# Kernel optimization log

Measured on AMD Instinct MI355X. Metric: run time of the kernel, lower is better.

Reference implementation:

```python
import jax, jax.numpy as jnp
import numpy as np

N, E, G = 30000, 240000, 1000
F, H = 78, 10            # in-features, GAT heads
HID = F * H              # 780
NEG_SLOPE = 0.2


def setup_inputs() -> dict:
    key = jax.random.key(0)
    ks = jax.random.split(key, 12)
    x = jax.random.normal(ks[0], (N, F), dtype=jnp.float32)
    edge_index = jax.random.randint(ks[1], (2, E), 0, N, dtype=jnp.int32)
    batch = jnp.sort(jax.random.randint(ks[2], (N,), 0, G, dtype=jnp.int32))
    def lin(k, fan_in, shape):
        return (jax.random.normal(k, shape, dtype=jnp.float32)
                / jnp.sqrt(jnp.float32(fan_in)))
    return {
        "x": x,
        "edge_index": edge_index,
        "batch": batch,
        "W_gat": lin(ks[3], F, (F, HID)),          # GATConv lin weight
        "att_src": lin(ks[4], F, (H, F)),          # GAT attention vectors
        "att_dst": lin(ks[5], F, (H, F)),
        "b_gat": jnp.zeros((HID,), jnp.float32),
        "W_gcn": lin(ks[6], HID, (HID, HID)),
        "b_gcn": jnp.zeros((HID,), jnp.float32),
        "W1": lin(ks[7], 2 * HID, (2 * HID, 1500)),
        "b1": jnp.zeros((1500,), jnp.float32),
        "W2": lin(ks[8], 1500, (1500, 128)),
        "b2": jnp.zeros((128,), jnp.float32),
    }


def _with_self_loops(edge_index):
    loop = jnp.arange(N, dtype=edge_index.dtype)
    src = jnp.concatenate([edge_index[0], loop])
    dst = jnp.concatenate([edge_index[1], loop])
    return src, dst


def reference(x, edge_index, batch, W_gat, att_src, att_dst, b_gat,
              W_gcn, b_gcn, W1, b1, W2, b2):
    src, dst = _with_self_loops(edge_index)  # [E+N]

    # ---- GATConv(78 -> 78, heads=10, concat) ----
    h = (x @ W_gat).reshape(N, H, F)                       # [N,H,F]
    a_src = jnp.einsum('nhf,hf->nh', h, att_src)           # [N,H]
    a_dst = jnp.einsum('nhf,hf->nh', h, att_dst)
    e = jax.nn.leaky_relu(a_src[src] + a_dst[dst], NEG_SLOPE)  # [Et,H]
    # segment softmax over incoming edges of each dst node
    e_max = jax.ops.segment_max(e, dst, num_segments=N)
    e_exp = jnp.exp(e - e_max[dst])
    denom = jax.ops.segment_sum(e_exp, dst, num_segments=N)
    alpha = e_exp / denom[dst]                             # [Et,H]
    msg = h[src] * alpha[:, :, None]                       # [Et,H,F]
    out = jax.ops.segment_sum(msg, dst, num_segments=N).reshape(N, HID) + b_gat
    out = jax.nn.relu(out)

    # ---- GCNConv(780 -> 780), symmetric norm with self loops ----
    h2 = out @ W_gcn                                       # [N,HID]
    deg = jax.ops.segment_sum(jnp.ones_like(dst, jnp.float32), dst,
                              num_segments=N)
    dinv = jax.lax.rsqrt(jnp.maximum(deg, 1.0))
    norm = dinv[src] * dinv[dst]                           # [Et]
    out2 = jax.ops.segment_sum(norm[:, None] * h2[src], dst,
                               num_segments=N) + b_gcn
    out2 = jax.nn.relu(out2)

    # ---- global mean / max pool over molecules ----
    counts = jax.ops.segment_sum(jnp.ones((N,), jnp.float32), batch,
                                 num_segments=G)
    gsum = jax.ops.segment_sum(out2, batch, num_segments=G)
    gmean = gsum / jnp.maximum(counts, 1.0)[:, None]
    gmax = jax.ops.segment_max(out2, batch, num_segments=G)
    gmax = jnp.where(counts[:, None] > 0, gmax, 0.0)
    pooled = jnp.concatenate([gmean, gmax], axis=1)        # [G, 1560]

    # ---- MLP head (dropout = identity at eval) ----
    hidfc = jax.nn.relu(pooled @ W1 + b1)
    return hidfc @ W2 + b2                                 # [G, 128]
```

## Files before the change

### kernel.cpp

```cpp
#include <hip/hip_runtime.h>

#define NN 30000
#define EE 240000
#define ET 270000
#define GG 1000
#define NH 10
#define FF 78
#define HID 780
#define NEG_SLOPE 0.2f

#define LD_H 784
#define KP_GCN 800
#define NP_HID 896
#define KP_X 96
#define MP_N 30080
#define KP_P 1600
#define NP_W1 1536
#define LD_FC 1536
#define MP_G 1024

#define MT 128
#define NT 128
#define NBLK 30
#define EB 4

#define C_X   (MP_N * KP_X)
#define C_WG  (NP_HID * KP_X)
#define C_WC  (NP_HID * KP_GCN)
#define C_W1  (NP_W1 * KP_P)
#define C_W2  (128 * LD_FC)
#define C_WS  (FF * 2 * NH)
#define C_IN  NN
#define C_TOT (C_X + C_WG + C_WC + C_W1 + C_W2 + C_WS + C_IN)

typedef __bf16 bf16_8 __attribute__((ext_vector_type(8)));
typedef float f32x4 __attribute__((ext_vector_type(4)));

__device__ __forceinline__ void async_copy16(const void* g, void* l) {
  __builtin_amdgcn_global_load_lds(
      (const __attribute__((address_space(1))) void*)g,
      (__attribute__((address_space(3))) void*)l, 16, 0, 0);
}

__device__ __forceinline__ float bf2f(unsigned int bits) {
  return __uint_as_float(bits << 16);
}

template <bool OUT_BF, int KBC, bool DBUF>
__global__ __launch_bounds__(256) void mfma_gemm(
    const __bf16* __restrict__ A, const __bf16* __restrict__ BT,
    float* __restrict__ Cf, __bf16* __restrict__ Cb,
    const float* __restrict__ bias, int M, int Kp, int Nout, int ldc,
    int relu, int rp, int nct, int mtiles) {
  constexpr int NST = KBC / 32;
  constexpr int TST = KBC / 16;
  constexpr int STAGEB = (KBC / 8) * MT * 8 * 2;
  __shared__ char smem[32768];
  int rt, ct;
  if (rp > 0) {
    int bid = blockIdx.x;
    int p = bid & 7, s = bid >> 3;
    int q = s / nct;
    rt = p * rp + q;
    ct = s - q * nct;
    if (rt >= mtiles) return;
  } else {
    rt = blockIdx.y; ct = blockIdx.x;
  }
  int row0 = rt * MT, col0 = ct * NT;
  int tid = threadIdx.x;
  int lane = tid & 63, wave = tid >> 6;
  int wm = (wave & 1) * 64, wn = (wave >> 1) * 64;
  int l15 = lane & 15, quad = lane >> 4;
  f32x4 acc[4][4] = {};

  auto stage = [&](int k0, int buf) {
    char* baseA = smem + (DBUF ? buf * 2 * STAGEB : 0);
    char* baseB = baseA + STAGEB;
    for (int t = 0; t < TST; t++) {
      int base = t * 256 + wave * 64;
      int s = base + lane;
      int kc = s >> 7, r = s & 127;
      async_copy16(A + (size_t)(row0 + r) * Kp + k0 + kc * 8,
                   baseA + (size_t)base * 16);
    }
    for (int t = 0; t < TST; t++) {
      int base = t * 256 + wave * 64;
      int s = base + lane;
      int kc = s >> 7, r = s & 127;
      async_copy16(BT + (size_t)(col0 + r) * Kp + k0 + kc * 8,
                   baseB + (size_t)base * 16);
    }
  };
  auto compute = [&](int buf) {
    char* baseA = smem + (DBUF ? buf * 2 * STAGEB : 0);
    char* baseB = baseA + STAGEB;
    for (int st = 0; st < NST; st++) {
      bf16_8 af[4], bfv[4];
      for (int mt = 0; mt < 4; mt++)
        af[mt] = *(const bf16_8*)(baseA +
            (size_t)((st * 4 + quad) * MT + wm + mt * 16 + l15) * 16);
      for (int nt = 0; nt < 4; nt++)
        bfv[nt] = *(const bf16_8*)(baseB +
            (size_t)((st * 4 + quad) * MT + wn + nt * 16 + l15) * 16);
      for (int mt = 0; mt < 4; mt++)
        for (int nt = 0; nt < 4; nt++)
          acc[mt][nt] = __builtin_amdgcn_mfma_f32_16x16x32_bf16(
              af[mt], bfv[nt], acc[mt][nt], 0, 0, 0);
    }
  };

  if (DBUF) {
    int niter = Kp / KBC;
    stage(0, 0);
    for (int k = 0; k < niter; k++) {
      __syncthreads();
      if (k + 1 < niter) stage((k + 1) * KBC, (k + 1) & 1);
      compute(k & 1);
    }
    __syncthreads();
  } else {
    for (int k0 = 0; k0 < Kp; k0 += KBC) {
      stage(k0, 0);
      __syncthreads();
      compute(0);
      __syncthreads();
    }
  }

  if (OUT_BF) {
    __bf16* Cs = (__bf16*)smem;
    for (int nt = 0; nt < 4; nt++) {
      int col_l = wn + nt * 16 + l15;
      int gcol = col0 + col_l;
      bool valid = gcol < Nout;
      float bv = (valid && bias) ? bias[gcol] : 0.f;
      int ch = col_l >> 3, wi = col_l & 7;
      for (int mt = 0; mt < 4; mt++) {
        for (int r = 0; r < 4; r++) {
          int rl = wm + mt * 16 + quad * 4 + r;
          float v = 0.f;
          if (valid) {
            v = acc[mt][nt][r] + bv;
            if (relu) v = fmaxf(v, 0.f);
          }
          Cs[rl * 128 + ((ch ^ (rl & 7)) << 3) + wi] = (__bf16)v;
        }
      }
    }
    __syncthreads();
    for (int idx = tid; idx < MT * 16; idx += 256) {
      int rl = idx >> 4, ch = idx & 15;
      int grow = row0 + rl, gcol = col0 + ch * 8;
      if (grow < M && gcol + 8 <= ldc)
        *(bf16_8*)(Cb + (size_t)grow * ldc + gcol) =
            *(const bf16_8*)&Cs[rl * 128 + ((ch ^ (rl & 7)) << 3)];
    }
  } else {
    for (int nt = 0; nt < 4; nt++) {
      int col = col0 + wn + nt * 16 + l15;
      if (col >= ldc) continue;
      bool valid = col < Nout;
      float bv = (valid && bias) ? bias[col] : 0.f;
      for (int mt = 0; mt < 4; mt++) {
        int rbase = row0 + wm + mt * 16 + quad * 4;
        for (int r = 0; r < 4; r++) {
          int row = rbase + r;
          if (row >= M) continue;
          float v = 0.f;
          if (valid) {
            v = acc[mt][nt][r] + bv;
            if (relu) v = fmaxf(v, 0.f);
          }
          Cf[(size_t)row * ldc + col] = v;
        }
      }
    }
  }
}

__global__ __launch_bounds__(256) void prep_kernel(
    const float* __restrict__ x, const float* __restrict__ W_gat,
    const float* __restrict__ att_src, const float* __restrict__ att_dst,
    const float* __restrict__ W_gcn, const float* __restrict__ W1,
    const float* __restrict__ W2, __bf16* __restrict__ x_bf,
    __bf16* __restrict__ WgatT, __bf16* __restrict__ WgcnT,
    __bf16* __restrict__ W1T, __bf16* __restrict__ W2T,
    float* __restrict__ wsd, int* __restrict__ cnt, int* __restrict__ fill,
    int* __restrict__ lo, int* __restrict__ hi) {
  int gid = blockIdx.x * 256 + threadIdx.x;
  if (gid < C_X) {
    int n = gid / KP_X, k = gid - n * KP_X;
    x_bf[gid] = (__bf16)((n < NN && k < FF) ? x[(size_t)n * FF + k] : 0.f);
    return;
  }
  gid -= C_X;
  if (gid < C_WG) {
    int n = gid / KP_X, k = gid - n * KP_X;
    WgatT[gid] = (__bf16)((n < HID && k < FF) ? W_gat[(size_t)k * HID + n] : 0.f);
    return;
  }
  gid -= C_WG;
  if (gid < C_WC) {
    int n = gid / KP_GCN, k = gid - n * KP_GCN;
    WgcnT[gid] = (__bf16)((n < HID && k < HID) ? W_gcn[(size_t)k * HID + n] : 0.f);
    return;
  }
  gid -= C_WC;
  if (gid < C_W1) {
    int n = gid / KP_P, k = gid - n * KP_P;
    W1T[gid] = (__bf16)((n < 1500 && k < 2 * HID) ? W1[(size_t)k * 1500 + n] : 0.f);
    return;
  }
  gid -= C_W1;
  if (gid < C_W2) {
    int n = gid / LD_FC, k = gid - n * LD_FC;
    W2T[gid] = (__bf16)((n < 128 && k < 1500) ? W2[(size_t)k * 128 + n] : 0.f);
    return;
  }
  gid -= C_W2;
  if (gid < C_WS) {
    int k = gid / (2 * NH), c = gid - k * (2 * NH);
    int h = (c < NH) ? c : c - NH;
    const float* att = (c < NH) ? att_src : att_dst;
    float s = 0.f;
    for (int f = 0; f < FF; f++)
      s += W_gat[(size_t)k * HID + h * FF + f] * att[h * FF + f];
    wsd[k * 2 * NH + c] = s;
    return;
  }
  gid -= C_WS;
  if (gid < C_IN) {
    cnt[gid] = 0; fill[gid] = 0;
    if (gid < GG) { lo[gid] = NN; hi[gid] = 0; }
  }
}

__device__ __forceinline__ void edge_sd(const int* __restrict__ ei, int t,
                                        int& s, int& d) {
  if (t < EE) { s = ei[t]; d = ei[EE + t]; }
  else        { s = t - EE; d = t - EE; }
}

__global__ __launch_bounds__(256) void adot_count_kernel(
    const float* __restrict__ x, const float* __restrict__ wsd,
    float* __restrict__ a_src, float* __restrict__ a_dst,
    const int* __restrict__ ei, const int* __restrict__ batch,
    int* __restrict__ cnt, int* __restrict__ lo, int* __restrict__ hi) {
  __shared__ float w_s[FF * 2 * NH];
  for (int i = threadIdx.x; i < FF * 2 * NH; i += 256) w_s[i] = wsd[i];
  int gid = blockIdx.x * 256 + threadIdx.x;
  if (gid < ET) { int s, d; edge_sd(ei, gid, s, d); atomicAdd(&cnt[d], 1); }
  if (gid < NN) {
    int g = batch[gid];
    atomicMin(&lo[g], gid);
    atomicMax(&hi[g], gid + 1);
  }
  __syncthreads();
  if (gid >= NN * 2 * NH) return;
  int n = gid / (2 * NH), c = gid - n * (2 * NH);
  float s = 0.f;
  for (int k = 0; k < FF; k++) s += x[(size_t)n * FF + k] * w_s[k * 2 * NH + c];
  if (c < NH) a_src[n * NH + c] = s;
  else        a_dst[n * NH + (c - NH)] = s;
}

__global__ __launch_bounds__(1024) void scan1_kernel(
    const int* __restrict__ cnt, int* __restrict__ row_ptr,
    int* __restrict__ partial) {
  __shared__ int buf[1024];
  int i = blockIdx.x * 1024 + threadIdx.x;
  int v = (i < NN) ? cnt[i] : 0;
  buf[threadIdx.x] = v;
  __syncthreads();
  for (int off = 1; off < 1024; off <<= 1) {
    int t = (threadIdx.x >= off) ? buf[threadIdx.x - off] : 0;
    __syncthreads();
    buf[threadIdx.x] += t;
    __syncthreads();
  }
  if (i < NN) row_ptr[i] = buf[threadIdx.x] - v;
  if (threadIdx.x == 1023) partial[blockIdx.x] = buf[1023];
}

__global__ __launch_bounds__(256) void scan3_kernel(
    int* __restrict__ row_ptr, const int* __restrict__ partial,
    const int* __restrict__ cnt, float* __restrict__ dinv) {
  __shared__ int pre[NBLK];
  if (threadIdx.x == 0) {
    int run = 0;
    for (int b = 0; b < NBLK; b++) { pre[b] = run; run += partial[b]; }
  }
  __syncthreads();
  int i = blockIdx.x * 256 + threadIdx.x;
  if (i < NN) {
    row_ptr[i] += pre[i >> 10];
    dinv[i] = rsqrtf((float)max(cnt[i], 1));
  }
  if (i == 0) row_ptr[NN] = ET;
}

__global__ void scatter_kernel(const int* __restrict__ ei,
                               const int* __restrict__ row_ptr,
                               int* __restrict__ fill,
                               const float* __restrict__ a_src,
                               const float* __restrict__ a_dst,
                               int* __restrict__ col_src,
                               float* __restrict__ p_csr) {
  int t = blockIdx.x * blockDim.x + threadIdx.x;
  if (t >= ET) return;
  int s, d; edge_sd(ei, t, s, d);
  int pos = row_ptr[d] + atomicAdd(&fill[d], 1);
  col_src[pos] = s;
#pragma unroll
  for (int h = 0; h < NH; h++) {
    float v = a_src[s * NH + h] + a_dst[d * NH + h];
    v = (v > 0.f) ? v : v * NEG_SLOPE;
    p_csr[(size_t)pos * NH + h] = __expf(v);
  }
}

__global__ __launch_bounds__(256) void gat_aggr_kernel(
    const int* __restrict__ row_ptr, const int* __restrict__ col_src,
    const float* __restrict__ p_csr, const __bf16* __restrict__ h_bf,
    const float* __restrict__ b_gat, __bf16* __restrict__ A_bf) {
  int wave = threadIdx.x >> 6;
  int lane = threadIdx.x & 63;
  int d = blockIdx.x * 2 + (wave >> 1);
  int half = wave & 1;
  int beg = row_ptr[d], end = row_ptr[d + 1];
  int f0 = half * 392 + 8 * lane;

  if (lane < 49) {
    int h0 = f0 / FF;
    int split = (h0 + 1) * FF - f0;
    if (split > 8) split = 8;
    int h1 = (h0 < NH - 1) ? h0 + 1 : NH - 1;
    float acc[8] = {};
    float sum0 = 0.f, sum1 = 0.f;
    for (int e = beg; e < end; e += EB) {
      int sidx[EB]; float pp0[EB], pp1[EB];
#pragma unroll
      for (int j = 0; j < EB; j++) {
        bool ok = (e + j < end);
        int ee = ok ? e + j : beg;
        sidx[j] = col_src[ee];
        float q0 = p_csr[(size_t)ee * NH + h0];
        float q1 = p_csr[(size_t)ee * NH + h1];
        pp0[j] = ok ? q0 : 0.f;
        pp1[j] = ok ? q1 : 0.f;
      }
      uint4 rr[EB];
#pragma unroll
      for (int j = 0; j < EB; j++)
        rr[j] = *(const uint4*)(h_bf + (size_t)sidx[j] * LD_H + f0);
#pragma unroll
      for (int j = 0; j < EB; j++) {
        sum0 += pp0[j]; sum1 += pp1[j];
        unsigned int w[4] = {rr[j].x, rr[j].y, rr[j].z, rr[j].w};
#pragma unroll
        for (int k = 0; k < 8; k++) {
          unsigned int bits = (k & 1) ? (w[k >> 1] >> 16) : (w[k >> 1] & 0xffffu);
          acc[k] += bf2f(bits) * ((k < split) ? pp0[j] : pp1[j]);
        }
      }
    }
    float inv0 = 1.f / sum0, inv1 = 1.f / sum1;
    bf16_8 o0;
#pragma unroll
    for (int k = 0; k < 8; k++) {
      int f = f0 + k;
      float val = 0.f;
      if (f < HID)
        val = fmaxf(acc[k] * ((k < split) ? inv0 : inv1) + b_gat[f], 0.f);
      o0[k] = (__bf16)val;
    }
    *(bf16_8*)(A_bf + (size_t)d * KP_GCN + f0) = o0;
  } else if (half == 1 && (lane == 49 || lane == 50)) {
    bf16_8 z = {};
    *(bf16_8*)(A_bf + (size_t)d * KP_GCN + 784 + (lane - 49) * 8) = z;
  }
}

__global__ __launch_bounds__(256) void gcn_aggr_kernel(
    const int* __restrict__ row_ptr, const int* __restrict__ col_src,
    const float* __restrict__ dinv, const __bf16* __restrict__ h2,
    const float* __restrict__ b_gcn, __bf16* __restrict__ out2) {
  int wave = threadIdx.x >> 6;
  int lane = threadIdx.x & 63;
  int d = blockIdx.x * 2 + (wave >> 1);
  int half = wave & 1;
  int beg = row_ptr[d], end = row_ptr[d + 1];
  if (lane >= 49) return;
  int f0 = half * 392 + 8 * lane;
  float dv = dinv[d];
  float acc[8] = {};
  for (int e = beg; e < end; e += EB) {
    int sidx[EB]; float ww[EB];
#pragma unroll
    for (int j = 0; j < EB; j++) {
      bool ok = (e + j < end);
      int ee = ok ? e + j : beg;
      int s = col_src[ee];
      sidx[j] = s;
      ww[j] = ok ? dinv[s] * dv : 0.f;
    }
    uint4 rr[EB];
#pragma unroll
    for (int j = 0; j < EB; j++)
      rr[j] = *(const uint4*)(h2 + (size_t)sidx[j] * LD_H + f0);
#pragma unroll
    for (int j = 0; j < EB; j++) {
      unsigned int wb[4] = {rr[j].x, rr[j].y, rr[j].z, rr[j].w};
#pragma unroll
      for (int k = 0; k < 8; k++) {
        unsigned int bits = (k & 1) ? (wb[k >> 1] >> 16) : (wb[k >> 1] & 0xffffu);
        acc[k] += bf2f(bits) * ww[j];
      }
    }
  }
  bf16_8 o0;
#pragma unroll
  for (int k = 0; k < 8; k++) {
    int f = f0 + k;
    float val = (f < HID) ? fmaxf(acc[k] + b_gcn[f], 0.f) : 0.f;
    o0[k] = (__bf16)val;
  }
  *(bf16_8*)(out2 + (size_t)d * LD_H + f0) = o0;
}

__global__ __launch_bounds__(128) void pool_kernel(
    const __bf16* __restrict__ out2, const int* __restrict__ lo,
    const int* __restrict__ hi, __bf16* __restrict__ pooled) {
  int g = blockIdx.x;
  int l = lo[g], h = hi[g];
  int t = threadIdx.x;
  if (t >= 98) {
    if (t < 103) {
      int base = 1560 + (t - 98) * 8;
      for (int k = 0; k < 8; k++) pooled[(size_t)g * KP_P + base + k] = (__bf16)0.f;
    }
    return;
  }
  int f0 = 8 * t;
  float s[8] = {}, mx[8];
#pragma unroll
  for (int k = 0; k < 8; k++) mx[k] = -1e30f;
  for (int n = l; n < h; n++) {
    uint4 r = *(const uint4*)(out2 + (size_t)n * LD_H + f0);
    unsigned int w[4] = {r.x, r.y, r.z, r.w};
#pragma unroll
    for (int k = 0; k < 8; k++) {
      unsigned int bits = (k & 1) ? (w[k >> 1] >> 16) : (w[k >> 1] & 0xffffu);
      float v = bf2f(bits);
      s[k] += v;
      mx[k] = fmaxf(mx[k], v);
    }
  }
  float invc = (h > l) ? 1.f / (float)(h - l) : 0.f;
#pragma unroll
  for (int k = 0; k < 8; k++) {
    int f = f0 + k;
    if (f >= HID) continue;
    float mean = (h > l) ? s[k] * invc : 0.f;
    float mxx  = (h > l) ? mx[k] : 0.f;
    pooled[(size_t)g * KP_P + f] = (__bf16)mean;
    pooled[(size_t)g * KP_P + HID + f] = (__bf16)mxx;
  }
}

extern "C" void kernel_launch(void* const* d_in, const int* in_sizes, int n_in,
                              void* d_out, int out_size, void* d_ws,
                              size_t ws_size, hipStream_t stream) {
  const float* x        = (const float*)d_in[0];
  const int*   edge_idx = (const int*)d_in[1];
  const int*   batch    = (const int*)d_in[2];
  const float* W_gat    = (const float*)d_in[3];
  const float* att_src  = (const float*)d_in[4];
  const float* att_dst  = (const float*)d_in[5];
  const float* b_gat    = (const float*)d_in[6];
  const float* W_gcn    = (const float*)d_in[7];
  const float* b_gcn    = (const float*)d_in[8];
  const float* W1       = (const float*)d_in[9];
  const float* b1       = (const float*)d_in[10];
  const float* W2       = (const float*)d_in[11];
  const float* b2       = (const float*)d_in[12];
  float* out = (float*)d_out;
  (void)in_sizes; (void)n_in; (void)out_size; (void)ws_size;

  char* ws = (char*)d_ws;
  size_t off = 0;
  auto alloc = [&](size_t bytes) -> void* {
    void* p = ws + off;
    off += (bytes + 255) & ~(size_t)255;
    return p;
  };
  char*  bufR     = (char*)alloc((size_t)MP_N * KP_GCN * 2);
  __bf16* A_bf    = (__bf16*)bufR;
  __bf16* out2b   = (__bf16*)bufR;
  __bf16* h_bf    = (__bf16*)alloc((size_t)MP_N * LD_H * 2);
  __bf16* h2_bf   = (__bf16*)alloc((size_t)MP_N * LD_H * 2);
  __bf16* x_bf    = (__bf16*)alloc((size_t)MP_N * KP_X * 2);
  __bf16* WgatT   = (__bf16*)alloc((size_t)NP_HID * KP_X * 2);
  __bf16* WgcnT   = (__bf16*)alloc((size_t)NP_HID * KP_GCN * 2);
  __bf16* W1T     = (__bf16*)alloc((size_t)NP_W1 * KP_P * 2);
  __bf16* W2T     = (__bf16*)alloc((size_t)128 * LD_FC * 2);
  __bf16* pooled  = (__bf16*)alloc((size_t)MP_G * KP_P * 2);
  __bf16* hidfc   = (__bf16*)alloc((size_t)MP_G * LD_FC * 2);
  float* wsd      = (float*)alloc((size_t)FF * 2 * NH * 4);
  float* a_src_b  = (float*)alloc((size_t)NN * NH * 4);
  float* a_dst_b  = (float*)alloc((size_t)NN * NH * 4);
  float* p_csr    = (float*)alloc((size_t)ET * NH * 4);
  int*   cnt      = (int*)alloc((size_t)NN * 4);
  int*   fill     = (int*)alloc((size_t)NN * 4);
  int*   row_ptr  = (int*)alloc((size_t)(NN + 1) * 4);
  int*   col_src  = (int*)alloc((size_t)ET * 4);
  int*   partial  = (int*)alloc((size_t)NBLK * 4);
  int*   lo       = (int*)alloc((size_t)GG * 4);
  int*   hi       = (int*)alloc((size_t)GG * 4);
  float* dinv     = (float*)alloc((size_t)NN * 4);

  prep_kernel<<<(C_TOT + 255) / 256, 256, 0, stream>>>(
      x, W_gat, att_src, att_dst, W_gcn, W1, W2, x_bf, WgatT, WgcnT, W1T, W2T,
      wsd, cnt, fill, lo, hi);

  {
    dim3 grid(NP_HID / NT, MP_N / MT);
    mfma_gemm<true, 32, true><<<grid, 256, 0, stream>>>(
        x_bf, WgatT, nullptr, h_bf, nullptr, NN, KP_X, HID, LD_H, 0, 0, 0, 0);
  }
  adot_count_kernel<<<(NN * 2 * NH + 255) / 256, 256, 0, stream>>>(
      x, wsd, a_src_b, a_dst_b, edge_idx, batch, cnt, lo, hi);

  scan1_kernel<<<NBLK, 1024, 0, stream>>>(cnt, row_ptr, partial);
  scan3_kernel<<<(NN + 255) / 256, 256, 0, stream>>>(row_ptr, partial, cnt,
                                                     dinv);
  scatter_kernel<<<(ET + 255) / 256, 256, 0, stream>>>(
      edge_idx, row_ptr, fill, a_src_b, a_dst_b, col_src, p_csr);

  gat_aggr_kernel<<<NN / 2, 256, 0, stream>>>(row_ptr, col_src, p_csr, h_bf,
                                              b_gat, A_bf);
  {
    mfma_gemm<true, 32, true><<<dim3(8 * 30 * 7), 256, 0, stream>>>(
        A_bf, WgcnT, nullptr, h2_bf, nullptr, NN, KP_GCN, HID, LD_H, 0,
        30, 7, MP_N / MT);
  }
  gcn_aggr_kernel<<<NN / 2, 256, 0, stream>>>(row_ptr, col_src, dinv, h2_bf,
                                              b_gcn, out2b);

  pool_kernel<<<GG, 128, 0, stream>>>(out2b, lo, hi, pooled);

  {
    dim3 grid(NP_W1 / NT, MP_G / MT);
    mfma_gemm<true, 64, false><<<grid, 256, 0, stream>>>(
        pooled, W1T, nullptr, hidfc, b1, GG, KP_P, 1500, LD_FC, 1, 0, 0, 0);
  }
  {
    dim3 grid(1, MP_G / MT);
    mfma_gemm<false, 64, false><<<grid, 256, 0, stream>>>(
        hidfc, W2T, out, nullptr, b2, GG, LD_FC, 128, 128, 0, 0, 0, 0);
  }
}
```

Baseline: 557.3 us.

## Aggregate raw features per head before GAT projection, then apply per-head GEMM

Uses linearity to reorder the GAT step: it first aggregates the 78-wide bf16 input features per head with the attention weights, then projects each head's aggregate through its own slice of W_gat in a new per-head MFMA GEMM that fuses bias and ReLU. The aim is to replace the gather of 780-wide projected rows per edge with gathers of 96-wide input rows. This removes the up-front x@W_gat GEMM but adds a 30000x960 intermediate and a separate head GEMM. The output layout pads each head to 80 columns, and W_gcn is repacked to match.

```diff
diff --git a/kernel.cpp b/kernel.cpp
--- a/kernel.cpp
+++ b/kernel.cpp
@@ -13,6 +13,7 @@
 #define KP_GCN 800
 #define NP_HID 896
 #define KP_X 96
+#define LD_Z 960
 #define MP_N 30080
 #define KP_P 1600
 #define NP_W1 1536
@@ -25,13 +26,14 @@
 #define EB 4
 
 #define C_X   (MP_N * KP_X)
-#define C_WG  (NP_HID * KP_X)
+#define C_WE  (NH * 128 * 96)
 #define C_WC  (NP_HID * KP_GCN)
 #define C_W1  (NP_W1 * KP_P)
 #define C_W2  (128 * LD_FC)
+#define C_PB  KP_GCN
 #define C_WS  (FF * 2 * NH)
 #define C_IN  NN
-#define C_TOT (C_X + C_WG + C_WC + C_W1 + C_W2 + C_WS + C_IN)
+#define C_TOT (C_X + C_WE + C_WC + C_W1 + C_W2 + C_PB + C_WS + C_IN)
 
 typedef __bf16 bf16_8 __attribute__((ext_vector_type(8)));
 typedef float f32x4 __attribute__((ext_vector_type(4)));
@@ -179,13 +181,82 @@
   }
 }
 
+__global__ __launch_bounds__(256) void gemm_head(
+    const __bf16* __restrict__ z, const __bf16* __restrict__ WE,
+    const float* __restrict__ pb, __bf16* __restrict__ C) {
+  __shared__ char smem[49152];
+  __bf16* As = (__bf16*)smem;
+  __bf16* Bs = (__bf16*)(smem + 24576);
+  int head = blockIdx.x;
+  int row0 = blockIdx.y * MT;
+  int col0 = 80 * head;
+  int tid = threadIdx.x;
+  int lane = tid & 63, wave = tid >> 6;
+  int wm = (wave & 1) * 64, wn = (wave >> 1) * 64;
+  int l15 = lane & 15, quad = lane >> 4;
+
+  for (int t = 0; t < 6; t++) {
+    int base = t * 256 + wave * 64;
+    int s = base + lane;
+    int kc = s >> 7, r = s & 127;
+    async_copy16(z + (size_t)(row0 + r) * LD_Z + 96 * head + kc * 8,
+                 (char*)As + (size_t)base * 16);
+  }
+  for (int t = 0; t < 6; t++) {
+    int base = t * 256 + wave * 64;
+    int s = base + lane;
+    int kc = s >> 7, r = s & 127;
+    async_copy16(WE + (size_t)head * 128 * 96 + (size_t)r * 96 + kc * 8,
+                 (char*)Bs + (size_t)base * 16);
+  }
+  __syncthreads();
+
+  f32x4 acc[4][4] = {};
+  for (int st = 0; st < 3; st++) {
+    bf16_8 af[4], bfv[4];
+    for (int mt = 0; mt < 4; mt++)
+      af[mt] = *(const bf16_8*)&As[(size_t)((st * 4 + quad) * 128 + wm + mt * 16 + l15) * 8];
+    for (int nt = 0; nt < 4; nt++)
+      bfv[nt] = *(const bf16_8*)&Bs[(size_t)((st * 4 + quad) * 128 + wn + nt * 16 + l15) * 8];
+    for (int mt = 0; mt < 4; mt++)
+      for (int nt = 0; nt < 4; nt++)
+        acc[mt][nt] = __builtin_amdgcn_mfma_f32_16x16x32_bf16(
+            af[mt], bfv[nt], acc[mt][nt], 0, 0, 0);
+  }
+  __syncthreads();
+
+  __bf16* Cs = (__bf16*)smem;
+  for (int nt = 0; nt < 4; nt++) {
+    int col_l = wn + nt * 16 + l15;
+    bool valid = col_l < 78;
+    float bv = valid ? pb[col0 + col_l] : 0.f;
+    int ch = col_l >> 3, wi = col_l & 7;
+    for (int mt = 0; mt < 4; mt++) {
+      for (int r = 0; r < 4; r++) {
+        int rl = wm + mt * 16 + quad * 4 + r;
+        float v = valid ? fmaxf(acc[mt][nt][r] + bv, 0.f) : 0.f;
+        Cs[rl * 128 + ((ch ^ (rl & 7)) << 3) + wi] = (__bf16)v;
+      }
+    }
+  }
+  __syncthreads();
+  for (int idx = tid; idx < MT * 10; idx += 256) {
+    int rl = idx / 10, ch = idx - rl * 10;
+    int grow = row0 + rl;
+    if (grow < NN)
+      *(bf16_8*)(C + (size_t)grow * KP_GCN + col0 + ch * 8) =
+          *(const bf16_8*)&Cs[rl * 128 + ((ch ^ (rl & 7)) << 3)];
+  }
+}
+
 __global__ __launch_bounds__(256) void prep_kernel(
     const float* __restrict__ x, const float* __restrict__ W_gat,
     const float* __restrict__ att_src, const float* __restrict__ att_dst,
     const float* __restrict__ W_gcn, const float* __restrict__ W1,
-    const float* __restrict__ W2, __bf16* __restrict__ x_bf,
-    __bf16* __restrict__ WgatT, __bf16* __restrict__ WgcnT,
-    __bf16* __restrict__ W1T, __bf16* __restrict__ W2T,
+    const float* __restrict__ W2, const float* __restrict__ b_gat,
+    __bf16* __restrict__ x_bf, __bf16* __restrict__ WE,
+    __bf16* __restrict__ WgcnT, __bf16* __restrict__ W1T,
+    __bf16* __restrict__ W2T, float* __restrict__ pb,
     float* __restrict__ wsd, int* __restrict__ cnt, int* __restrict__ fill,
     int* __restrict__ lo, int* __restrict__ hi) {
   int gid = blockIdx.x * 256 + threadIdx.x;
@@ -195,15 +266,20 @@
     return;
   }
   gid -= C_X;
-  if (gid < C_WG) {
-    int n = gid / KP_X, k = gid - n * KP_X;
-    WgatT[gid] = (__bf16)((n < HID && k < FF) ? W_gat[(size_t)k * HID + n] : 0.f);
-    return;
-  }
-  gid -= C_WG;
+  if (gid < C_WE) {
+    int h = gid / (128 * 96);
+    int rem = gid - h * 128 * 96;
+    int n = rem / 96, k = rem - n * 96;
+    WE[gid] = (__bf16)((n < FF && k < FF)
+                           ? W_gat[(size_t)k * HID + h * FF + n] : 0.f);
+    return;
+  }
+  gid -= C_WE;
   if (gid < C_WC) {
-    int n = gid / KP_GCN, k = gid - n * KP_GCN;
-    WgcnT[gid] = (__bf16)((n < HID && k < HID) ? W_gcn[(size_t)k * HID + n] : 0.f);
+    int n = gid / KP_GCN, kp = gid - n * KP_GCN;
+    int hh = kp / 80, f = kp - hh * 80;
+    WgcnT[gid] = (__bf16)((n < HID && f < FF)
+                              ? W_gcn[(size_t)(FF * hh + f) * HID + n] : 0.f);
     return;
   }
   gid -= C_WC;
@@ -219,6 +295,12 @@
     return;
   }
   gid -= C_W2;
+  if (gid < C_PB) {
+    int hh = gid / 80, f = gid - hh * 80;
+    pb[gid] = (f < FF) ? b_gat[FF * hh + f] : 0.f;
+    return;
+  }
+  gid -= C_PB;
   if (gid < C_WS) {
     int k = gid / (2 * NH), c = gid - k * (2 * NH);
     int h = (c < NH) ? c : c - NH;
@@ -320,65 +402,60 @@
   }
 }
 
-__global__ __launch_bounds__(256) void gat_aggr_kernel(
+__global__ __launch_bounds__(256) void gat_x_aggr_kernel(
     const int* __restrict__ row_ptr, const int* __restrict__ col_src,
-    const float* __restrict__ p_csr, const __bf16* __restrict__ h_bf,
-    const float* __restrict__ b_gat, __bf16* __restrict__ A_bf) {
+    const float* __restrict__ p_csr, const __bf16* __restrict__ x_bf,
+    __bf16* __restrict__ z) {
   int wave = threadIdx.x >> 6;
   int lane = threadIdx.x & 63;
   int d = blockIdx.x * 2 + (wave >> 1);
-  int half = wave & 1;
+  int idx = (wave & 1) * 64 + lane;
   int beg = row_ptr[d], end = row_ptr[d + 1];
-  int f0 = half * 392 + 8 * lane;
-
-  if (lane < 49) {
-    int h0 = f0 / FF;
-    int split = (h0 + 1) * FF - f0;
-    if (split > 8) split = 8;
-    int h1 = (h0 < NH - 1) ? h0 + 1 : NH - 1;
+
+  if (idx < 100) {
+    int h = idx / 10, j = idx - h * 10;
+    int k0 = 8 * j;
     float acc[8] = {};
-    float sum0 = 0.f, sum1 = 0.f;
+    float sum = 0.f;
     for (int e = beg; e < end; e += EB) {
-      int sidx[EB]; float pp0[EB], pp1[EB];
-#pragma unroll
-      for (int j = 0; j < EB; j++) {
-        bool ok = (e + j < end);
-        int ee = ok ? e + j : beg;
-        sidx[j] = col_src[ee];
-        float q0 = p_csr[(size_t)ee * NH + h0];
-        float q1 = p_csr[(size_t)ee * NH + h1];
-        pp0[j] = ok ? q0 : 0.f;
-        pp1[j] = ok ? q1 : 0.f;
+      int sidx[EB]; float pp[EB];
+#pragma unroll
+      for (int q = 0; q < EB; q++) {
+        bool ok = (e + q < end);
+        int ee = ok ? e + q : beg;
+        sidx[q] = col_src[ee];
+        float p = p_csr[(size_t)ee * NH + h];
+        pp[q] = ok ? p : 0.f;
       }
       uint4 rr[EB];
 #pragma unroll
-      for (int j = 0; j < EB; j++)
-        rr[j] = *(const uint4*)(h_bf + (size_t)sidx[j] * LD_H + f0);
-#pragma unroll
-      for (int j = 0; j < EB; j++) {
-        sum0 += pp0[j]; sum1 += pp1[j];
-        unsigned int w[4] = {rr[j].x, rr[j].y, rr[j].z, rr[j].w};
+      for (int q = 0; q < EB; q++)
+        rr[q] = *(const uint4*)(x_bf + (size_t)sidx[q] * KP_X + k0);
+#pragma unroll
+      for (int q = 0; q < EB; q++) {
+        sum += pp[q];
+        unsigned int w[4] = {rr[q].x, rr[q].y, rr[q].z, rr[q].w};
 #pragma unroll
         for (int k = 0; k < 8; k++) {
           unsigned int bits = (k & 1) ? (w[k >> 1] >> 16) : (w[k >> 1] & 0xffffu);
-          acc[k] += bf2f(bits) * ((k < split) ? pp0[j] : pp1[j]);
+          acc[k] += bf2f(bits) * pp[q];
         }
       }
     }
-    float inv0 = 1.f / sum0, inv1 = 1.f / sum1;
-    bf16_8 o0;
+    float inv = 1.f / sum;
+    bf16_8 o;
 #pragma unroll
     for (int k = 0; k < 8; k++) {
-      int f = f0 + k;
-      float val = 0.f;
-      if (f < HID)
-        val = fmaxf(acc[k] * ((k < split) ? inv0 : inv1) + b_gat[f], 0.f);
-      o0[k] = (__bf16)val;
-    }
-    *(bf16_8*)(A_bf + (size_t)d * KP_GCN + f0) = o0;
-  } else if (half == 1 && (lane == 49 || lane == 50)) {
-    bf16_8 z = {};
-    *(bf16_8*)(A_bf + (size_t)d * KP_GCN + 784 + (lane - 49) * 8) = z;
+      float val = (k0 + k < FF) ? acc[k] * inv : 0.f;
+      o[k] = (__bf16)val;
+    }
+    *(bf16_8*)(z + (size_t)d * LD_Z + 96 * h + k0) = o;
+  } else if (idx < 120) {
+    int t = idx - 100;
+    int h = t >> 1;
+    int k0 = 80 + 8 * (t & 1);
+    bf16_8 zz = {};
+    *(bf16_8*)(z + (size_t)d * LD_Z + 96 * h + k0) = zz;
   }
 }
 
@@ -498,15 +575,16 @@
   char*  bufR     = (char*)alloc((size_t)MP_N * KP_GCN * 2);
   __bf16* A_bf    = (__bf16*)bufR;
   __bf16* out2b   = (__bf16*)bufR;
-  __bf16* h_bf    = (__bf16*)alloc((size_t)MP_N * LD_H * 2);
+  __bf16* z_bf    = (__bf16*)alloc((size_t)MP_N * LD_Z * 2);
   __bf16* h2_bf   = (__bf16*)alloc((size_t)MP_N * LD_H * 2);
   __bf16* x_bf    = (__bf16*)alloc((size_t)MP_N * KP_X * 2);
-  __bf16* WgatT   = (__bf16*)alloc((size_t)NP_HID * KP_X * 2);
+  __bf16* WE      = (__bf16*)alloc((size_t)NH * 128 * 96 * 2);
   __bf16* WgcnT   = (__bf16*)alloc((size_t)NP_HID * KP_GCN * 2);
   __bf16* W1T     = (__bf16*)alloc((size_t)NP_W1 * KP_P * 2);
   __bf16* W2T     = (__bf16*)alloc((size_t)128 * LD_FC * 2);
   __bf16* pooled  = (__bf16*)alloc((size_t)MP_G * KP_P * 2);
   __bf16* hidfc   = (__bf16*)alloc((size_t)MP_G * LD_FC * 2);
+  float* pb       = (float*)alloc((size_t)KP_GCN * 4);
   float* wsd      = (float*)alloc((size_t)FF * 2 * NH * 4);
   float* a_src_b  = (float*)alloc((size_t)NN * NH * 4);
   float* a_dst_b  = (float*)alloc((size_t)NN * NH * 4);
@@ -521,14 +599,9 @@
   float* dinv     = (float*)alloc((size_t)NN * 4);
 
   prep_kernel<<<(C_TOT + 255) / 256, 256, 0, stream>>>(
-      x, W_gat, att_src, att_dst, W_gcn, W1, W2, x_bf, WgatT, WgcnT, W1T, W2T,
-      wsd, cnt, fill, lo, hi);
-
-  {
-    dim3 grid(NP_HID / NT, MP_N / MT);
-    mfma_gemm<true, 32, true><<<grid, 256, 0, stream>>>(
-        x_bf, WgatT, nullptr, h_bf, nullptr, NN, KP_X, HID, LD_H, 0, 0, 0, 0);
-  }
+      x, W_gat, att_src, att_dst, W_gcn, W1, W2, b_gat, x_bf, WE, WgcnT, W1T,
+      W2T, pb, wsd, cnt, fill, lo, hi);
+
   adot_count_kernel<<<(NN * 2 * NH + 255) / 256, 256, 0, stream>>>(
       x, wsd, a_src_b, a_dst_b, edge_idx, batch, cnt, lo, hi);
 
@@ -538,8 +611,9 @@
   scatter_kernel<<<(ET + 255) / 256, 256, 0, stream>>>(
       edge_idx, row_ptr, fill, a_src_b, a_dst_b, col_src, p_csr);
 
-  gat_aggr_kernel<<<NN / 2, 256, 0, stream>>>(row_ptr, col_src, p_csr, h_bf,
-                                              b_gat, A_bf);
+  gat_x_aggr_kernel<<<NN / 2, 256, 0, stream>>>(row_ptr, col_src, p_csr, x_bf,
+                                                z_bf);
+  gemm_head<<<dim3(NH, MP_N / MT), 256, 0, stream>>>(z_bf, WE, pb, A_bf);
   {
     mfma_gemm<true, 32, true><<<dim3(8 * 30 * 7), 256, 0, stream>>>(
         A_bf, WgcnT, nullptr, h2_bf, nullptr, NN, KP_GCN, HID, LD_H, 0,
```

Result: faster. 537.3 us (-3.6%).
